# Optimization experiments

Hardware: AMD Instinct MI355X
Metric: run time of the kernel (lower is better)

## Reference

```python
import jax, jax.numpy as jnp
import numpy as np

D_MODEL = 1024
NUM_HEADS = 16
NUM_KV_HEADS = 4
D_K = D_MODEL // NUM_HEADS          # 64
GROUP = NUM_HEADS // NUM_KV_HEADS   # 4
D_KV = D_MODEL // GROUP             # 256


def setup_inputs() -> dict:
    key = jax.random.key(0)
    ks = jax.random.split(key, 12)
    B, S = 2, 2048
    sc = 0.02
    return {
        "query": jax.random.normal(ks[0], (B, S, D_MODEL), jnp.float32),
        "key": jax.random.normal(ks[1], (B, S, D_MODEL), jnp.float32),
        "value": jax.random.normal(ks[2], (B, S, D_MODEL), jnp.float32),
        "w_q": jax.random.normal(ks[3], (D_MODEL, D_MODEL), jnp.float32) * sc,
        "b_q": jnp.zeros((D_MODEL,), jnp.float32),
        "w_k": jax.random.normal(ks[4], (D_KV, D_MODEL), jnp.float32) * sc,
        "b_k": jnp.zeros((D_KV,), jnp.float32),
        "w_v": jax.random.normal(ks[5], (D_KV, D_MODEL), jnp.float32) * sc,
        "b_v": jnp.zeros((D_KV,), jnp.float32),
        "w_o": jax.random.normal(ks[6], (D_MODEL, D_MODEL), jnp.float32) * sc,
        "b_o": jnp.zeros((D_MODEL,), jnp.float32),
    }


def reference(query, key, value, w_q, b_q, w_k, b_k, w_v, b_v, w_o, b_o):
    B, S, _ = query.shape
    # projections (torch Linear: x @ W.T + b)
    Q = query @ w_q.T + b_q            # [B,S,d_model]
    K = key @ w_k.T + b_k              # [B,S,d_kv]
    V = value @ w_v.T + b_v            # [B,S,d_kv]
    # [B, Hkv, G, S, Dk] for Q; [B, Hkv, S, Dk] for K/V.
    # repeat_interleave(group, dim=1) on K/V == sharing each KV head across
    # its group of query heads, so we contract without duplicating K/V.
    Q = Q.reshape(B, S, NUM_KV_HEADS, GROUP, D_K).transpose(0, 2, 3, 1, 4)
    K = K.reshape(B, S, NUM_KV_HEADS, D_K).transpose(0, 2, 1, 3)
    V = V.reshape(B, S, NUM_KV_HEADS, D_K).transpose(0, 2, 1, 3)
    scale = 1.0 / jnp.sqrt(jnp.asarray(D_K, Q.dtype))
    scores = jnp.einsum('bhgsd,bhtd->bhgst', Q, K) * scale  # [B,Hkv,G,S,S]
    attn = jax.nn.softmax(scores, axis=-1)
    out = jnp.einsum('bhgst,bhtd->bhgsd', attn, V)          # [B,Hkv,G,S,Dk]
    # -> [B,S,Hkv*G*Dk] = [B,S,d_model]
    out = out.transpose(0, 3, 1, 2, 4).reshape(B, S, D_MODEL)
    return out @ w_o.T + b_o
```

## Files before the change

### kernel.cpp

```cpp
#include <hip/hip_runtime.h>
#include <hip/hip_bf16.h>
#include <stdint.h>

typedef unsigned short u16;
typedef unsigned int   u32;
typedef short s16x8 __attribute__((ext_vector_type(8)));
typedef u16   u16x4 __attribute__((ext_vector_type(4)));
typedef u16   u16x8 __attribute__((ext_vector_type(8)));
typedef u32   u32x2 __attribute__((ext_vector_type(2)));
typedef u32   u32x4 __attribute__((ext_vector_type(4)));
typedef float f32x4  __attribute__((ext_vector_type(4)));
typedef float f32x16 __attribute__((ext_vector_type(16)));
typedef float f4     __attribute__((ext_vector_type(4)));

#define MFMA(a,b,c)   __builtin_amdgcn_mfma_f32_16x16x32_bf16((a),(b),(c),0,0,0)
#define MFMA32(a,b,c) __builtin_amdgcn_mfma_f32_32x32x16_bf16((a),(b),(c),0,0,0)

#define BAR()   __builtin_amdgcn_s_barrier()
#define SCHED() __builtin_amdgcn_sched_barrier(0)

__device__ __forceinline__ u16 f2b(float f){
  union { float f; unsigned u; } v; v.f = f;
  unsigned r = v.u + 0x7fffu + ((v.u >> 16) & 1u);
  return (u16)(r >> 16);
}

__device__ __forceinline__ u32 cvtpk(float lo, float hi){
  u32 r;
  asm("v_cvt_pk_bf16_f32 %0, %1, %2" : "=v"(r) : "v"(lo), "v"(hi));
  return r;
}

__device__ __forceinline__ float exp2h(float x){
  float r;
  asm("v_exp_f32 %0, %1" : "=v"(r) : "v"(x));
  return r;
}

__device__ __forceinline__ void gll16(const void* g, void* l){
  __builtin_amdgcn_global_load_lds(
      (const __attribute__((address_space(1))) void*)g,
      (__attribute__((address_space(3))) void*)l, 16, 0, 0);
}

__global__ __launch_bounds__(256) void wcast(const float* __restrict__ wq,
                                             const float* __restrict__ wk,
                                             const float* __restrict__ wv,
                                             const float* __restrict__ wo,
                                             u16* dq, u16* dk, u16* dv, u16* dov){
  int e = (blockIdx.x * 256 + threadIdx.x) * 4;
  const float* s; u16* d; int off;
  if      (e < 1048576){ s = wq; d = dq;  off = 0; }
  else if (e < 1310720){ s = wk; d = dk;  off = 1048576; }
  else if (e < 1572864){ s = wv; d = dv;  off = 1310720; }
  else                 { s = wo; d = dov; off = 1572864; }
  int i = e - off;
  f4 v = *(const f4*)(s + i);
  u32x2 o; o[0] = cvtpk(v[0], v[1]); o[1] = cvtpk(v[2], v[3]);
  *(u32x2*)(d + i) = o;
}

__global__ __launch_bounds__(256) void qkv_gemm(
    const float* __restrict__ qa, const float* __restrict__ ka, const float* __restrict__ va,
    const u16* __restrict__ wq, const u16* __restrict__ wk, const u16* __restrict__ wv,
    const float* __restrict__ bq, const float* __restrict__ bk, const float* __restrict__ bv,
    u16* Qo, u16* Ko, u16* Vto){
  __shared__ float Asf[3][64*32];
  __shared__ u16   Bsw[3][128*32];
  const int tid = threadIdx.x, lane = tid & 63, wid = tid >> 6;
  const int lb = (blockIdx.x & 7) * 96 + (blockIdx.x >> 3);
  const float* A; const u16* B; const float* bias; int N; float cscale; int bm, bn;
  bool isV = false;
  if (lb < 512)      { A=qa; B=wq; bias=bq; N=1024; cscale=0.18033688011112f; bm=lb>>3;       bn=lb&7; }
  else if (lb < 640) { A=ka; B=wk; bias=bk; N=256;  cscale=1.0f;              bm=(lb-512)>>1; bn=(lb-512)&1; }
  else               { A=va; B=wv; bias=bv; N=256;  cscale=1.0f;              bm=(lb-640)>>1; bn=(lb-640)&1; isV = true; }
  const int wr = wid >> 1, wc = wid & 1;
  const int r15 = lane & 15, kg = lane >> 4;

  const u16*   Bg = B + (size_t)bn * 128 * 1024;
  const float* Ag = A + (size_t)bm * 64 * 1024;
  f32x4 acc[2][4] = {};

  auto stage = [&](int buf, int k0){
    #pragma unroll
    for (int i = 0; i < 2; i++){
      int cc = wid + i*4;
      int brow = cc*16 + (lane >> 2);
      int bslot = (lane & 3) ^ ((brow >> 1) & 3);
      gll16((const char*)Bg + (size_t)brow*2048 + k0*2 + bslot*16,
            (char*)&Bsw[buf][0] + cc*1024);
      int arow = cc*8 + (lane >> 3);
      int aslot = (lane & 7) ^ (arow & 7);
      gll16((const char*)Ag + (size_t)arow*4096 + k0*4 + aslot*16,
            (char*)&Asf[buf][0] + cc*1024);
    }
  };

  auto compute = [&](int buf){
    s16x8 af[2], bf[4];
    #pragma unroll
    for (int i = 0; i < 2; i++){
      int row = wr*32 + i*16 + r15;
      const char* rb = (const char*)&Asf[buf][0] + row*128;
      f4 va_ = *(const f4*)(rb + ((((kg*2)    ) ^ (row & 7)) << 4));
      f4 vb_ = *(const f4*)(rb + ((((kg*2) + 1) ^ (row & 7)) << 4));
      u32x4 o; o[0]=cvtpk(va_[0],va_[1]); o[1]=cvtpk(va_[2],va_[3]);
               o[2]=cvtpk(vb_[0],vb_[1]); o[3]=cvtpk(vb_[2],vb_[3]);
      af[i] = *(const s16x8*)&o;
    }
    #pragma unroll
    for (int j = 0; j < 4; j++){
      int row = wc*64 + j*16 + r15;
      bf[j] = *(const s16x8*)((const char*)&Bsw[buf][0] + row*64 + ((kg ^ ((row >> 1) & 3)) << 4));
    }
    __builtin_amdgcn_s_setprio(1);
    #pragma unroll
    for (int i = 0; i < 2; i++)
      #pragma unroll
      for (int j = 0; j < 4; j++)
        acc[i][j] = MFMA(af[i], bf[j], acc[i][j]);
    __builtin_amdgcn_s_setprio(0);
  };

  stage(0, 0); stage(1, 32); stage(2, 64);
  int bsel = 0;
  for (int t = 0; t < 29; t++){
    asm volatile("s_waitcnt vmcnt(8)" ::: "memory");
    BAR(); SCHED();
    compute(bsel);
    SCHED(); BAR();
    stage(bsel, (t + 3)*32);
    bsel = (bsel == 2) ? 0 : bsel + 1;
  }
  asm volatile("s_waitcnt vmcnt(8)" ::: "memory");
  BAR(); SCHED();
  compute(bsel);
  bsel = (bsel == 2) ? 0 : bsel + 1;
  asm volatile("s_waitcnt vmcnt(4)" ::: "memory");
  BAR(); SCHED();
  compute(bsel);
  bsel = (bsel == 2) ? 0 : bsel + 1;
  asm volatile("s_waitcnt vmcnt(0)" ::: "memory");
  BAR(); SCHED();
  compute(bsel);

  if (isV){
    #pragma unroll
    for (int i = 0; i < 2; i++){
      int row0 = bm*64 + wr*32 + i*16 + kg*4;
      int bb = row0 >> 11, t = row0 & 2047;
      #pragma unroll
      for (int j = 0; j < 4; j++){
        int col = bn*128 + wc*64 + j*16 + r15;
        float bj = bias[col];
        u16x4 vv;
        #pragma unroll
        for (int r = 0; r < 4; r++) vv[r] = f2b(acc[i][j][r] + bj);
        *(u16x4*)&Vto[((size_t)(bb*256 + col) << 11) + t] = vv;
      }
    }
  } else {
    u16* C = (lb < 512) ? Qo : Ko;
    #pragma unroll
    for (int i = 0; i < 2; i++){
      int row = bm*64 + wr*32 + i*16 + kg*4;
      #pragma unroll
      for (int j = 0; j < 4; j++){
        int col = bn*128 + wc*64 + j*16 + r15;
        float bj = bias[col];
        #pragma unroll
        for (int r = 0; r < 4; r++)
          C[(size_t)(row + r)*N + col] = f2b((acc[i][j][r] + bj) * cscale);
      }
    }
  }
}

__global__ __launch_bounds__(256) void gemm_o(const u16* __restrict__ Aw,
                                              const u16* __restrict__ Bw,
                                              const float* __restrict__ bias,
                                              float* __restrict__ Cv){
  __shared__ u16 As[3][64*32];
  __shared__ u16 Bs[3][128*32];
  const int tid = threadIdx.x, lane = tid & 63, wid = tid >> 6;
  const int lb = (blockIdx.x & 7) * 64 + (blockIdx.x >> 3);
  const int bm = lb >> 3, bn = lb & 7;
  const int wr = wid >> 1, wc = wid & 1;
  const int r15 = lane & 15, kg = lane >> 4;
  const u16* Ag = Aw + (size_t)bm * 64 * 1024;
  const u16* Bg = Bw + (size_t)bn * 128 * 1024;
  f32x4 acc[2][4] = {};

  auto stage = [&](int buf, int k0){
    int arow = wid*16 + (lane >> 2);
    int aslot = (lane & 3) ^ ((arow >> 1) & 3);
    gll16((const char*)Ag + (size_t)arow*2048 + k0*2 + aslot*16,
          (char*)&As[buf][0] + wid*1024);
    #pragma unroll
    for (int i = 0; i < 2; i++){
      int cc = wid + i*4;
      int brow = cc*16 + (lane >> 2);
      int bslot = (lane & 3) ^ ((brow >> 1) & 3);
      gll16((const char*)Bg + (size_t)brow*2048 + k0*2 + bslot*16,
            (char*)&Bs[buf][0] + cc*1024);
    }
  };

  auto compute = [&](int buf){
    s16x8 af[2], bf[4];
    #pragma unroll
    for (int i = 0; i < 2; i++){
      int row = wr*32 + i*16 + r15;
      af[i] = *(const s16x8*)((const char*)&As[buf][0] + row*64 + ((kg ^ ((row >> 1) & 3)) << 4));
    }
    #pragma unroll
    for (int j = 0; j < 4; j++){
      int row = wc*64 + j*16 + r15;
      bf[j] = *(const s16x8*)((const char*)&Bs[buf][0] + row*64 + ((kg ^ ((row >> 1) & 3)) << 4));
    }
    __builtin_amdgcn_s_setprio(1);
    #pragma unroll
    for (int i = 0; i < 2; i++)
      #pragma unroll
      for (int j = 0; j < 4; j++)
        acc[i][j] = MFMA(af[i], bf[j], acc[i][j]);
    __builtin_amdgcn_s_setprio(0);
  };

  stage(0, 0); stage(1, 32); stage(2, 64);
  int bsel = 0;
  for (int t = 0; t < 29; t++){
    asm volatile("s_waitcnt vmcnt(6)" ::: "memory");
    BAR(); SCHED();
    compute(bsel);
    SCHED(); BAR();
    stage(bsel, (t + 3)*32);
    bsel = (bsel == 2) ? 0 : bsel + 1;
  }
  asm volatile("s_waitcnt vmcnt(6)" ::: "memory");
  BAR(); SCHED();
  compute(bsel);
  bsel = (bsel == 2) ? 0 : bsel + 1;
  asm volatile("s_waitcnt vmcnt(3)" ::: "memory");
  BAR(); SCHED();
  compute(bsel);
  bsel = (bsel == 2) ? 0 : bsel + 1;
  asm volatile("s_waitcnt vmcnt(0)" ::: "memory");
  BAR(); SCHED();
  compute(bsel);

  #pragma unroll
  for (int i = 0; i < 2; i++){
    int row = bm*64 + wr*32 + i*16 + kg*4;
    #pragma unroll
    for (int j = 0; j < 4; j++){
      int col = bn*128 + wc*64 + j*16 + r15;
      float bj = bias[col];
      #pragma unroll
      for (int r = 0; r < 4; r++)
        Cv[(size_t)(row + r)*1024 + col] = acc[i][j][r] + bj;
    }
  }
}

__global__ __launch_bounds__(512, 4) void attn_fwd(const u16* __restrict__ Qp,
                                                   const u16* __restrict__ Kp,
                                                   const u16* __restrict__ Vt,
                                                   u16* __restrict__ Op){
  __shared__ u16 Ks[2][2][64*64];
  __shared__ u16 Vs[2][2][64*64];
  const int tid = threadIdx.x, lane = tid & 63, w = tid >> 6;
  const int wg = w & 3, g = w >> 2;
  const int bx = blockIdx.x;
  const int qt = bx & 15, h = (bx >> 4) & 15, b = bx >> 8;
  const int kvh = h >> 2;
  const int l31 = lane & 31, hh = lane >> 5;
  const int srow = lane >> 3;
  const int scol16 = ((lane & 7) ^ srow) << 4;

  const size_t qrow0 = (size_t)(b*2048 + qt*128 + wg*32 + l31) << 10;
  s16x8 qf[4];
  #pragma unroll
  for (int db = 0; db < 4; db++)
    qf[db] = *(const s16x8*)(Qp + qrow0 + h*64 + db*16 + hh*8);

  f32x16 oacc[2] = {};
  const f32x16 ZERO = {};
  float lsum = 0.f;

  auto stage = [&](int buf, int t0){
    #pragma unroll
    for (int i = 0; i < 2; i++){
      int cc = wg + i*4;
      int row = cc*8 + srow;
      const u16* ksrc = Kp + ((size_t)(b*2048 + t0 + row) << 8) + kvh*64;
      gll16((const char*)ksrc + scol16, (char*)&Ks[g][buf][0] + cc*1024);
      const u16* vsrc = Vt + ((size_t)((b*4 + kvh)*64 + row) << 11) + t0;
      gll16((const char*)vsrc + scol16, (char*)&Vs[g][buf][0] + cc*1024);
    }
  };

  stage(0, g*64);

  for (int it = 0; it < 16; it++){
    const int cur = it & 1;
    if (it + 1 < 16){
      stage(cur ^ 1, (2*(it + 1) + g)*64);
      asm volatile("s_waitcnt vmcnt(4)" ::: "memory");
    } else {
      asm volatile("s_waitcnt vmcnt(0)" ::: "memory");
    }
    BAR(); SCHED();

    f32x16 sacc[2];
    __builtin_amdgcn_s_setprio(1);
    #pragma unroll
    for (int kb2 = 0; kb2 < 2; kb2++){
      #pragma unroll
      for (int db = 0; db < 4; db++){
        int row = kb2*32 + l31;
        int slot = (db*2 + hh) ^ (row & 7);
        s16x8 kf = *(const s16x8*)((const char*)&Ks[g][cur][0] + row*128 + slot*16);
        sacc[kb2] = MFMA32(kf, qf[db], (db == 0) ? ZERO : sacc[kb2]);
      }
    }
    __builtin_amdgcn_s_setprio(0);

    u32 W[2][4][2];
    #pragma unroll
    for (int kb2 = 0; kb2 < 2; kb2++){
      float p[16];
      #pragma unroll
      for (int r = 0; r < 16; r++){
        p[r] = exp2h(sacc[kb2][r]);
        lsum += p[r];
      }
      #pragma unroll
      for (int a = 0; a < 4; a++){
        W[kb2][a][0] = cvtpk(p[4*a + 0], p[4*a + 1]);
        W[kb2][a][1] = cvtpk(p[4*a + 2], p[4*a + 3]);
      }
    }

    s16x8 pa[4];
    #pragma unroll
    for (int kq = 0; kq < 4; kq++){
      const int kb2 = kq >> 1, c = kq & 1;
      u32x4 dw;
      #pragma unroll
      for (int pp = 0; pp < 2; pp++){
        u32 x = W[kb2][2*c][pp], y = W[kb2][2*c + 1][pp];
        asm volatile("v_permlane32_swap_b32 %0, %1" : "+v"(x), "+v"(y));
        dw[pp] = x; dw[2 + pp] = y;
      }
      pa[kq] = *(const s16x8*)&dw;
    }

    __builtin_amdgcn_s_setprio(1);
    #pragma unroll
    for (int dblk = 0; dblk < 2; dblk++){
      #pragma unroll
      for (int kq = 0; kq < 4; kq++){
        int row = dblk*32 + l31;
        int slot = (kq*2 + hh) ^ (row & 7);
        s16x8 vf = *(const s16x8*)((const char*)&Vs[g][cur][0] + row*128 + slot*16);
        oacc[dblk] = MFMA32(pa[kq], vf, oacc[dblk]);
      }
    }
    __builtin_amdgcn_s_setprio(0);
    SCHED(); BAR();
  }
  __syncthreads();

  float rsum = lsum + __shfl_xor(lsum, 32, 64);
  float* Om = (float*)&Ks[0][0][0];
  float* Ls = (float*)&Vs[0][0][0];
  if (g == 1){
    #pragma unroll
    for (int reg = 0; reg < 16; reg++){
      int q = (reg & 3) + 4*hh + 8*(reg >> 2);
      #pragma unroll
      for (int dblk = 0; dblk < 2; dblk++)
        Om[(wg*32 + q)*64 + dblk*32 + l31] = oacc[dblk][reg];
    }
    if (hh == 0) Ls[wg*32 + l31] = rsum;
  }
  __syncthreads();
  if (g == 0){
    rsum += Ls[wg*32 + l31];
    float rinv = __builtin_amdgcn_rcpf(rsum);
    const size_t obase = (size_t)(b*2048 + qt*128 + wg*32) << 10;
    #pragma unroll
    for (int reg = 0; reg < 16; reg++){
      const int qrow = (reg & 3) + 4*hh + 8*(reg >> 2);
      float rq = __shfl(rinv, qrow, 64);
      #pragma unroll
      for (int dblk = 0; dblk < 2; dblk++){
        float v = (oacc[dblk][reg] + Om[(wg*32 + qrow)*64 + dblk*32 + l31]) * rq;
        Op[obase + ((size_t)qrow << 10) + h*64 + dblk*32 + l31] = f2b(v);
      }
    }
  }
}

extern "C" void kernel_launch(void* const* d_in, const int* in_sizes, int n_in,
                              void* d_out, int out_size, void* d_ws, size_t ws_size,
                              hipStream_t stream){
  const float* query = (const float*)d_in[0];
  const float* key   = (const float*)d_in[1];
  const float* value = (const float*)d_in[2];
  const float* w_q   = (const float*)d_in[3];
  const float* b_q   = (const float*)d_in[4];
  const float* w_k   = (const float*)d_in[5];
  const float* b_k   = (const float*)d_in[6];
  const float* w_v   = (const float*)d_in[7];
  const float* b_v   = (const float*)d_in[8];
  const float* w_o   = (const float*)d_in[9];
  const float* b_o   = (const float*)d_in[10];

  char* ws = (char*)d_ws;
  size_t off = 0;
  u16* wqb = (u16*)(ws + off); off += (size_t)1024*1024*2;
  u16* wkb = (u16*)(ws + off); off += (size_t)256*1024*2;
  u16* wvb = (u16*)(ws + off); off += (size_t)256*1024*2;
  u16* wob = (u16*)(ws + off); off += (size_t)1024*1024*2;
  u16* Qw  = (u16*)(ws + off); off += (size_t)4096*1024*2;
  u16* Kw  = (u16*)(ws + off); off += (size_t)4096*256*2;
  u16* Vtw = (u16*)(ws + off); off += (size_t)4096*256*2;
  u16* AOw = (u16*)(ws + off); off += (size_t)4096*1024*2;

  wcast<<<2560, 256, 0, stream>>>(w_q, w_k, w_v, w_o, wqb, wkb, wvb, wob);

  qkv_gemm<<<768, 256, 0, stream>>>(query, key, value, wqb, wkb, wvb,
                                    b_q, b_k, b_v, Qw, Kw, Vtw);

  attn_fwd<<<512, 512, 0, stream>>>(Qw, Kw, Vtw, AOw);

  gemm_o<<<512, 256, 0, stream>>>(AOw, wob, b_o, (float*)d_out);
}
```

Measured before the change: 97.75 us.

## Pre-cast activations to bf16 and enlarge QKV GEMM tiles with BK=64

The activation fp32-to-bf16 conversion moves out of the QKV GEMM into the cast kernel, which now also converts query, key and value into workspace buffers (query reuses the attention-output buffer). The QKV GEMM changes to 128x128 tiles with K-step 64 and double buffering, halving its grid. The output GEMM also moves to K-step 64 double buffering. This aims to cut per-iteration overhead and raise MFMA density, at the cost of an extra full round trip of activations through memory and fewer blocks in flight.

Measured after the change: 97.22 us. Within noise of the previous version (-0.5%).

```diff
diff --git a/kernel.cpp b/kernel.cpp
--- a/kernel.cpp
+++ b/kernel.cpp
@@ -6,8 +6,6 @@
 typedef unsigned int   u32;
 typedef short s16x8 __attribute__((ext_vector_type(8)));
 typedef u16   u16x4 __attribute__((ext_vector_type(4)));
-typedef u16   u16x8 __attribute__((ext_vector_type(8)));
-typedef u32   u32x2 __attribute__((ext_vector_type(2)));
 typedef u32   u32x4 __attribute__((ext_vector_type(4)));
 typedef float f32x4  __attribute__((ext_vector_type(4)));
 typedef float f32x16 __attribute__((ext_vector_type(16)));
@@ -43,111 +41,105 @@
       (__attribute__((address_space(3))) void*)l, 16, 0, 0);
 }
 
-__global__ __launch_bounds__(256) void wcast(const float* __restrict__ wq,
-                                             const float* __restrict__ wk,
-                                             const float* __restrict__ wv,
-                                             const float* __restrict__ wo,
-                                             u16* dq, u16* dk, u16* dv, u16* dov){
-  int e = (blockIdx.x * 256 + threadIdx.x) * 4;
-  const float* s; u16* d; int off;
-  if      (e < 1048576){ s = wq; d = dq;  off = 0; }
-  else if (e < 1310720){ s = wk; d = dk;  off = 1048576; }
-  else if (e < 1572864){ s = wv; d = dv;  off = 1310720; }
-  else                 { s = wo; d = dov; off = 1572864; }
-  int i = e - off;
-  f4 v = *(const f4*)(s + i);
-  u32x2 o; o[0] = cvtpk(v[0], v[1]); o[1] = cvtpk(v[2], v[3]);
-  *(u32x2*)(d + i) = o;
+__global__ __launch_bounds__(256) void wcast8(
+    const float* __restrict__ q,  const float* __restrict__ k,  const float* __restrict__ v,
+    const float* __restrict__ wq, const float* __restrict__ wk, const float* __restrict__ wv,
+    const float* __restrict__ wo,
+    u16* qb, u16* kb, u16* vb, u16* dq, u16* dk, u16* dv, u16* dov){
+  const int bx = blockIdx.x;
+  const float* s; u16* d; int base;
+  if      (bx < 2048){ s = q;  d = qb;  base = bx; }
+  else if (bx < 4096){ s = k;  d = kb;  base = bx - 2048; }
+  else if (bx < 6144){ s = v;  d = vb;  base = bx - 4096; }
+  else if (bx < 6656){ s = wq; d = dq;  base = bx - 6144; }
+  else if (bx < 6784){ s = wk; d = dk;  base = bx - 6656; }
+  else if (bx < 6912){ s = wv; d = dv;  base = bx - 6784; }
+  else               { s = wo; d = dov; base = bx - 6912; }
+  int i = base*2048 + threadIdx.x*8;
+  f4 v0 = *(const f4*)(s + i);
+  f4 v1 = *(const f4*)(s + i + 4);
+  u32x4 o; o[0] = cvtpk(v0[0], v0[1]); o[1] = cvtpk(v0[2], v0[3]);
+           o[2] = cvtpk(v1[0], v1[1]); o[3] = cvtpk(v1[2], v1[3]);
+  *(u32x4*)(d + i) = o;
 }
 
 __global__ __launch_bounds__(256) void qkv_gemm(
-    const float* __restrict__ qa, const float* __restrict__ ka, const float* __restrict__ va,
+    const u16* __restrict__ qa, const u16* __restrict__ ka, const u16* __restrict__ va,
     const u16* __restrict__ wq, const u16* __restrict__ wk, const u16* __restrict__ wv,
     const float* __restrict__ bq, const float* __restrict__ bk, const float* __restrict__ bv,
     u16* Qo, u16* Ko, u16* Vto){
-  __shared__ float Asf[3][64*32];
-  __shared__ u16   Bsw[3][128*32];
+  __shared__ u16 As[2][128*64];
+  __shared__ u16 Bs[2][128*64];
   const int tid = threadIdx.x, lane = tid & 63, wid = tid >> 6;
-  const int lb = (blockIdx.x & 7) * 96 + (blockIdx.x >> 3);
-  const float* A; const u16* B; const float* bias; int N; float cscale; int bm, bn;
+  const int lb = (blockIdx.x & 7) * 48 + (blockIdx.x >> 3);
+  const u16* A; const u16* B; const float* bias; int N; float cscale; int bm, bn;
   bool isV = false;
-  if (lb < 512)      { A=qa; B=wq; bias=bq; N=1024; cscale=0.18033688011112f; bm=lb>>3;       bn=lb&7; }
-  else if (lb < 640) { A=ka; B=wk; bias=bk; N=256;  cscale=1.0f;              bm=(lb-512)>>1; bn=(lb-512)&1; }
-  else               { A=va; B=wv; bias=bv; N=256;  cscale=1.0f;              bm=(lb-640)>>1; bn=(lb-640)&1; isV = true; }
+  if (lb < 256)      { A=qa; B=wq; bias=bq; N=1024; cscale=0.18033688011112f; bm=lb>>3;       bn=lb&7; }
+  else if (lb < 320) { A=ka; B=wk; bias=bk; N=256;  cscale=1.0f;              bm=(lb-256)>>1; bn=(lb-256)&1; }
+  else               { A=va; B=wv; bias=bv; N=256;  cscale=1.0f;              bm=(lb-320)>>1; bn=(lb-320)&1; isV = true; }
   const int wr = wid >> 1, wc = wid & 1;
   const int r15 = lane & 15, kg = lane >> 4;
 
-  const u16*   Bg = B + (size_t)bn * 128 * 1024;
-  const float* Ag = A + (size_t)bm * 64 * 1024;
-  f32x4 acc[2][4] = {};
+  const u16* Ag = A + (size_t)bm * 128 * 1024;
+  const u16* Bg = B + (size_t)bn * 128 * 1024;
+  f32x4 acc[4][4] = {};
+
+  const int rr = lane >> 3;
+  const int slot16 = ((lane & 7) ^ rr) << 4;
 
   auto stage = [&](int buf, int k0){
     #pragma unroll
-    for (int i = 0; i < 2; i++){
+    for (int i = 0; i < 4; i++){
       int cc = wid + i*4;
-      int brow = cc*16 + (lane >> 2);
-      int bslot = (lane & 3) ^ ((brow >> 1) & 3);
-      gll16((const char*)Bg + (size_t)brow*2048 + k0*2 + bslot*16,
-            (char*)&Bsw[buf][0] + cc*1024);
-      int arow = cc*8 + (lane >> 3);
-      int aslot = (lane & 7) ^ (arow & 7);
-      gll16((const char*)Ag + (size_t)arow*4096 + k0*4 + aslot*16,
-            (char*)&Asf[buf][0] + cc*1024);
+      size_t rowoff = (size_t)(cc*8 + rr) * 2048 + (size_t)k0 * 2;
+      gll16((const char*)Ag + rowoff + slot16, (char*)&As[buf][0] + cc*1024);
+      gll16((const char*)Bg + rowoff + slot16, (char*)&Bs[buf][0] + cc*1024);
     }
   };
 
   auto compute = [&](int buf){
-    s16x8 af[2], bf[4];
-    #pragma unroll
-    for (int i = 0; i < 2; i++){
-      int row = wr*32 + i*16 + r15;
-      const char* rb = (const char*)&Asf[buf][0] + row*128;
-      f4 va_ = *(const f4*)(rb + ((((kg*2)    ) ^ (row & 7)) << 4));
-      f4 vb_ = *(const f4*)(rb + ((((kg*2) + 1) ^ (row & 7)) << 4));
-      u32x4 o; o[0]=cvtpk(va_[0],va_[1]); o[1]=cvtpk(va_[2],va_[3]);
-               o[2]=cvtpk(vb_[0],vb_[1]); o[3]=cvtpk(vb_[2],vb_[3]);
-      af[i] = *(const s16x8*)&o;
-    }
-    #pragma unroll
-    for (int j = 0; j < 4; j++){
-      int row = wc*64 + j*16 + r15;
-      bf[j] = *(const s16x8*)((const char*)&Bsw[buf][0] + row*64 + ((kg ^ ((row >> 1) & 3)) << 4));
-    }
-    __builtin_amdgcn_s_setprio(1);
-    #pragma unroll
-    for (int i = 0; i < 2; i++)
-      #pragma unroll
-      for (int j = 0; j < 4; j++)
-        acc[i][j] = MFMA(af[i], bf[j], acc[i][j]);
-    __builtin_amdgcn_s_setprio(0);
+    #pragma unroll
+    for (int h = 0; h < 2; h++){
+      s16x8 af[4], bf[4];
+      #pragma unroll
+      for (int i = 0; i < 4; i++){
+        int row = wr*64 + i*16 + r15;
+        af[i] = *(const s16x8*)((const char*)&As[buf][0] + row*128 + (((h*4 + kg) ^ (row & 7)) << 4));
+      }
+      #pragma unroll
+      for (int j = 0; j < 4; j++){
+        int row = wc*64 + j*16 + r15;
+        bf[j] = *(const s16x8*)((const char*)&Bs[buf][0] + row*128 + (((h*4 + kg) ^ (row & 7)) << 4));
+      }
+      __builtin_amdgcn_s_setprio(1);
+      #pragma unroll
+      for (int i = 0; i < 4; i++)
+        #pragma unroll
+        for (int j = 0; j < 4; j++)
+          acc[i][j] = MFMA(af[i], bf[j], acc[i][j]);
+      __builtin_amdgcn_s_setprio(0);
+    }
   };
 
-  stage(0, 0); stage(1, 32); stage(2, 64);
-  int bsel = 0;
-  for (int t = 0; t < 29; t++){
+  stage(0, 0); stage(1, 64);
+  for (int t = 0; t < 14; t++){
     asm volatile("s_waitcnt vmcnt(8)" ::: "memory");
     BAR(); SCHED();
-    compute(bsel);
+    compute(t & 1);
     SCHED(); BAR();
-    stage(bsel, (t + 3)*32);
-    bsel = (bsel == 2) ? 0 : bsel + 1;
+    stage(t & 1, (t + 2)*64);
   }
   asm volatile("s_waitcnt vmcnt(8)" ::: "memory");
   BAR(); SCHED();
-  compute(bsel);
-  bsel = (bsel == 2) ? 0 : bsel + 1;
-  asm volatile("s_waitcnt vmcnt(4)" ::: "memory");
-  BAR(); SCHED();
-  compute(bsel);
-  bsel = (bsel == 2) ? 0 : bsel + 1;
+  compute(0);
   asm volatile("s_waitcnt vmcnt(0)" ::: "memory");
   BAR(); SCHED();
-  compute(bsel);
+  compute(1);
 
   if (isV){
     #pragma unroll
-    for (int i = 0; i < 2; i++){
-      int row0 = bm*64 + wr*32 + i*16 + kg*4;
+    for (int i = 0; i < 4; i++){
+      int row0 = bm*128 + wr*64 + i*16 + kg*4;
       int bb = row0 >> 11, t = row0 & 2047;
       #pragma unroll
       for (int j = 0; j < 4; j++){
@@ -160,10 +152,10 @@
       }
     }
   } else {
-    u16* C = (lb < 512) ? Qo : Ko;
-    #pragma unroll
-    for (int i = 0; i < 2; i++){
-      int row = bm*64 + wr*32 + i*16 + kg*4;
+    u16* C = (lb < 256) ? Qo : Ko;
+    #pragma unroll
+    for (int i = 0; i < 4; i++){
+      int row = bm*128 + wr*64 + i*16 + kg*4;
       #pragma unroll
       for (int j = 0; j < 4; j++){
         int col = bn*128 + wc*64 + j*16 + r15;
@@ -180,8 +172,8 @@
                                               const u16* __restrict__ Bw,
                                               const float* __restrict__ bias,
                                               float* __restrict__ Cv){
-  __shared__ u16 As[3][64*32];
-  __shared__ u16 Bs[3][128*32];
+  __shared__ u16 As[2][64*64];
+  __shared__ u16 Bs[2][128*64];
   const int tid = threadIdx.x, lane = tid & 63, wid = tid >> 6;
   const int lb = (blockIdx.x & 7) * 64 + (blockIdx.x >> 3);
   const int bm = lb >> 3, bn = lb & 7;
@@ -191,63 +183,62 @@
   const u16* Bg = Bw + (size_t)bn * 128 * 1024;
   f32x4 acc[2][4] = {};
 
+  const int rr = lane >> 3;
+  const int slot16 = ((lane & 7) ^ rr) << 4;
+
   auto stage = [&](int buf, int k0){
-    int arow = wid*16 + (lane >> 2);
-    int aslot = (lane & 3) ^ ((arow >> 1) & 3);
-    gll16((const char*)Ag + (size_t)arow*2048 + k0*2 + aslot*16,
-          (char*)&As[buf][0] + wid*1024);
     #pragma unroll
     for (int i = 0; i < 2; i++){
       int cc = wid + i*4;
-      int brow = cc*16 + (lane >> 2);
-      int bslot = (lane & 3) ^ ((brow >> 1) & 3);
-      gll16((const char*)Bg + (size_t)brow*2048 + k0*2 + bslot*16,
-            (char*)&Bs[buf][0] + cc*1024);
+      size_t rowoff = (size_t)(cc*8 + rr) * 2048 + (size_t)k0 * 2;
+      gll16((const char*)Ag + rowoff + slot16, (char*)&As[buf][0] + cc*1024);
+    }
+    #pragma unroll
+    for (int i = 0; i < 4; i++){
+      int cc = wid + i*4;
+      size_t rowoff = (size_t)(cc*8 + rr) * 2048 + (size_t)k0 * 2;
+      gll16((const char*)Bg + rowoff + slot16, (char*)&Bs[buf][0] + cc*1024);
     }
   };
 
   auto compute = [&](int buf){
-    s16x8 af[2], bf[4];
-    #pragma unroll
-    for (int i = 0; i < 2; i++){
-      int row = wr*32 + i*16 + r15;
-      af[i] = *(const s16x8*)((const char*)&As[buf][0] + row*64 + ((kg ^ ((row >> 1) & 3)) << 4));
-    }
-    #pragma unroll
-    for (int j = 0; j < 4; j++){
-      int row = wc*64 + j*16 + r15;
-      bf[j] = *(const s16x8*)((const char*)&Bs[buf][0] + row*64 + ((kg ^ ((row >> 1) & 3)) << 4));
-    }
-    __builtin_amdgcn_s_setprio(1);
-    #pragma unroll
-    for (int i = 0; i < 2; i++)
-      #pragma unroll
-      for (int j = 0; j < 4; j++)
-        acc[i][j] = MFMA(af[i], bf[j], acc[i][j]);
-    __builtin_amdgcn_s_setprio(0);
+    #pragma unroll
+    for (int h = 0; h < 2; h++){
+      s16x8 af[2], bf[4];
+      #pragma unroll
+      for (int i = 0; i < 2; i++){
+        int row = wr*32 + i*16 + r15;
+        af[i] = *(const s16x8*)((const char*)&As[buf][0] + row*128 + (((h*4 + kg) ^ (row & 7)) << 4));
+      }
+      #pragma unroll
+      for (int j = 0; j < 4; j++){
+        int row = wc*64 + j*16 + r15;
+        bf[j] = *(const s16x8*)((const char*)&Bs[buf][0] + row*128 + (((h*4 + kg) ^ (row & 7)) << 4));
+      }
+      __builtin_amdgcn_s_setprio(1);
+      #pragma unroll
+      for (int i = 0; i < 2; i++)
+        #pragma unroll
+        for (int j = 0; j < 4; j++)
+          acc[i][j] = MFMA(af[i], bf[j], acc[i][j]);
+      __builtin_amdgcn_s_setprio(0);
+    }
   };
 
-  stage(0, 0); stage(1, 32); stage(2, 64);
-  int bsel = 0;
-  for (int t = 0; t < 29; t++){
+  stage(0, 0); stage(1, 64);
+  for (int t = 0; t < 14; t++){
     asm volatile("s_waitcnt vmcnt(6)" ::: "memory");
     BAR(); SCHED();
-    compute(bsel);
+    compute(t & 1);
     SCHED(); BAR();
-    stage(bsel, (t + 3)*32);
-    bsel = (bsel == 2) ? 0 : bsel + 1;
+    stage(t & 1, (t + 2)*64);
   }
   asm volatile("s_waitcnt vmcnt(6)" ::: "memory");
   BAR(); SCHED();
-  compute(bsel);
-  bsel = (bsel == 2) ? 0 : bsel + 1;
-  asm volatile("s_waitcnt vmcnt(3)" ::: "memory");
-  BAR(); SCHED();
-  compute(bsel);
-  bsel = (bsel == 2) ? 0 : bsel + 1;
+  compute(0);
   asm volatile("s_waitcnt vmcnt(0)" ::: "memory");
   BAR(); SCHED();
-  compute(bsel);
+  compute(1);
 
   #pragma unroll
   for (int i = 0; i < 2; i++){
@@ -428,10 +419,14 @@
   u16* Kw  = (u16*)(ws + off); off += (size_t)4096*256*2;
   u16* Vtw = (u16*)(ws + off); off += (size_t)4096*256*2;
   u16* AOw = (u16*)(ws + off); off += (size_t)4096*1024*2;
-
-  wcast<<<2560, 256, 0, stream>>>(w_q, w_k, w_v, w_o, wqb, wkb, wvb, wob);
-
-  qkv_gemm<<<768, 256, 0, stream>>>(query, key, value, wqb, wkb, wvb,
+  u16* kb  = (u16*)(ws + off); off += (size_t)4096*1024*2;
+  u16* vb  = (u16*)(ws + off); off += (size_t)4096*1024*2;
+  u16* qb  = AOw;
+
+  wcast8<<<7424, 256, 0, stream>>>(query, key, value, w_q, w_k, w_v, w_o,
+                                   qb, kb, vb, wqb, wkb, wvb, wob);
+
+  qkv_gemm<<<384, 256, 0, stream>>>(qb, kb, vb, wqb, wkb, wvb,
                                     b_q, b_k, b_v, Qw, Kw, Vtw);
 
   attn_fwd<<<512, 512, 0, stream>>>(Qw, Kw, Vtw, AOw);
```
